# Kernel tuning notes

Hardware: AMD Instinct MI355X
Metric: run time of the kernel (lower is better)

## Reference

```python
import jax, jax.numpy as jnp
import numpy as np

EPS = 1e-6

def setup_inputs() -> dict:
    key = jax.random.key(0)
    ks = jax.random.split(key, 4)
    T, B, D, N = 512, 16, 1024, 512
    # xavier-uniform-ish scale for projections
    lim = float(np.sqrt(6.0 / (N + D)))
    x = jax.random.normal(ks[0], (T, B, D), dtype=jnp.float32)
    W_k = jax.random.uniform(ks[1], (N, D), minval=-lim, maxval=lim, dtype=jnp.float32)
    W_v = jax.random.uniform(ks[2], (N, D), minval=-lim, maxval=lim, dtype=jnp.float32)
    W_q = jax.random.uniform(ks[3], (N, D), minval=-lim, maxval=lim, dtype=jnp.float32)
    return {"x": x, "W_k": W_k, "W_v": W_v, "W_q": W_q}

def reference(x, W_k, W_v, W_q):
    # x: (T, B, D); delta-rule fast-weight cell, proj=no_z, nonlin=tanh,
    # gate=output, update=delta.
    T, B, D = x.shape
    n = W_k.shape[0]
    k = jnp.einsum('tbd,nd->tbn', x, W_k)
    v = jnp.einsum('tbd,nd->tbn', x, W_v)
    q = jnp.einsum('tbd,nd->tbn', x, W_q)
    k_norm = k / (jnp.linalg.norm(k, axis=-1, keepdims=True) + EPS)

    def step(S, kvq):
        k_t, v_t, q_t = kvq  # each (B, n)
        retrieved = jnp.einsum('bij,bj->bi', S, k_t)
        delta = v_t - retrieved
        S_new = jnp.tanh(S + delta[:, :, None] * k_t[:, None, :])
        Sq = jnp.einsum('bij,bj->bi', S_new, q_t)
        out = Sq * jax.nn.silu(Sq)
        return S_new, out

    S0 = jnp.zeros((B, n, n), dtype=x.dtype)
    S_final, outputs = jax.lax.scan(step, S0, (k_norm, v, q))
    return outputs, S_final
```

## Files before the change

### kernel.cpp

```cpp
#include <hip/hip_runtime.h>
#include <hip/hip_bf16.h>

#define T_DIM 512
#define B_DIM 16
#define D_DIM 1024
#define N_DIM 512

#define C_FOLD  2.885390082f
#define INV_C   0.3465735903f

typedef short s16x8 __attribute__((ext_vector_type(8)));
typedef float f32x4 __attribute__((ext_vector_type(4)));
typedef float f32x2 __attribute__((ext_vector_type(2)));

__device__ __forceinline__ unsigned short f2bf(float f) {
    unsigned u = __float_as_uint(f);
    unsigned r = (u + 0x7fffu + ((u >> 16) & 1u)) >> 16;
    return (unsigned short)r;
}

__device__ __forceinline__ float half32_sum(float x) {
    x += __int_as_float(__builtin_amdgcn_update_dpp(0, __float_as_int(x), 0xB1,  0xf, 0xf, true));
    x += __int_as_float(__builtin_amdgcn_update_dpp(0, __float_as_int(x), 0x4E,  0xf, 0xf, true));
    x += __int_as_float(__builtin_amdgcn_update_dpp(0, __float_as_int(x), 0x124, 0xf, 0xf, true));
    x += __int_as_float(__builtin_amdgcn_update_dpp(0, __float_as_int(x), 0x128, 0xf, 0xf, true));
    x += __int_as_float(__builtin_amdgcn_ds_swizzle(__float_as_int(x), 0x401F));
    return x;
}

__global__ __launch_bounds__(256) void proj_gemm(
    const float* __restrict__ x,
    const float* __restrict__ Wk,
    const float* __restrict__ Wv,
    const float* __restrict__ Wq,
    float* __restrict__ kbuf, float* __restrict__ vbuf, float* __restrict__ qbuf)
{
    const float* W = (blockIdx.z == 0) ? Wk : (blockIdx.z == 1) ? Wv : Wq;
    float* out = (blockIdx.z == 0) ? kbuf : (blockIdx.z == 1) ? vbuf : qbuf;

    __shared__ __align__(16) unsigned short As[64 * 40];
    __shared__ __align__(16) unsigned short Bs[64 * 40];

    const int tid  = threadIdx.x;
    const int m0   = blockIdx.x * 64;
    const int n0   = blockIdx.y * 64;
    const int wave = tid >> 6;
    const int lane = tid & 63;
    const int l15  = lane & 15;
    const int quad = lane >> 4;

    const int srow = tid >> 2;
    const int scol = (tid & 3) * 8;

    f32x4 acc[4];
#pragma unroll
    for (int i = 0; i < 4; ++i) acc[i] = (f32x4)0.0f;

    for (int k0 = 0; k0 < D_DIM; k0 += 32) {
        __syncthreads();
        {
            const float* srcA = &x[(size_t)(m0 + srow) * D_DIM + k0 + scol];
            float4 a0 = *(const float4*)srcA;
            float4 a1 = *(const float4*)(srcA + 4);
            uint4 pa;
            pa.x = (unsigned)f2bf(a0.x) | ((unsigned)f2bf(a0.y) << 16);
            pa.y = (unsigned)f2bf(a0.z) | ((unsigned)f2bf(a0.w) << 16);
            pa.z = (unsigned)f2bf(a1.x) | ((unsigned)f2bf(a1.y) << 16);
            pa.w = (unsigned)f2bf(a1.z) | ((unsigned)f2bf(a1.w) << 16);
            *(uint4*)&As[srow * 40 + scol] = pa;

            const float* srcB = &W[(size_t)(n0 + srow) * D_DIM + k0 + scol];
            float4 b0 = *(const float4*)srcB;
            float4 b1 = *(const float4*)(srcB + 4);
            uint4 pb;
            pb.x = (unsigned)f2bf(b0.x) | ((unsigned)f2bf(b0.y) << 16);
            pb.y = (unsigned)f2bf(b0.z) | ((unsigned)f2bf(b0.w) << 16);
            pb.z = (unsigned)f2bf(b1.x) | ((unsigned)f2bf(b1.y) << 16);
            pb.w = (unsigned)f2bf(b1.z) | ((unsigned)f2bf(b1.w) << 16);
            *(uint4*)&Bs[srow * 40 + scol] = pb;
        }
        __syncthreads();
        s16x8 af = *(const s16x8*)&As[(wave * 16 + l15) * 40 + quad * 8];
#pragma unroll
        for (int nt = 0; nt < 4; ++nt) {
            s16x8 bf = *(const s16x8*)&Bs[(nt * 16 + l15) * 40 + quad * 8];
            acc[nt] = __builtin_amdgcn_mfma_f32_16x16x32_bf16(af, bf, acc[nt], 0, 0, 0);
        }
    }
#pragma unroll
    for (int nt = 0; nt < 4; ++nt) {
#pragma unroll
        for (int rg = 0; rg < 4; ++rg) {
            int row = m0 + wave * 16 + quad * 4 + rg;
            int col = n0 + nt * 16 + l15;
            out[(size_t)row * N_DIM + col] = acc[nt][rg];
        }
    }
}

__global__ __launch_bounds__(256) void knorm(float* __restrict__ kbuf)
{
    const int wave = threadIdx.x >> 6;
    const int lane = threadIdx.x & 63;
    const int row  = blockIdx.x * 4 + wave;
    float* p = &kbuf[(size_t)row * N_DIM + lane * 8];
    float4 a = *(const float4*)p;
    float4 b = *(const float4*)(p + 4);
    float s = a.x*a.x + a.y*a.y + a.z*a.z + a.w*a.w
            + b.x*b.x + b.y*b.y + b.z*b.z + b.w*b.w;
#pragma unroll
    for (int m = 1; m < 64; m <<= 1) s += __shfl_xor(s, m, 64);
    float inv = 1.0f / (sqrtf(s) + 1e-6f);
    a.x *= inv; a.y *= inv; a.z *= inv; a.w *= inv;
    b.x *= inv; b.y *= inv; b.z *= inv; b.w *= inv;
    *(float4*)p = a;
    *(float4*)(p + 4) = b;
}

__global__ __launch_bounds__(256) void scan_kernel(
    const float* __restrict__ kbuf, const float* __restrict__ vbuf,
    const float* __restrict__ qbuf, float* __restrict__ out)
{
    __shared__ __align__(16) float ks[2][576];
    __shared__ __align__(16) float qs[2][576];
    __shared__ float vs[2][16];

    const int tid  = threadIdx.x;
    const int lane = tid & 63;
    const int wv   = tid >> 6;
    const int h    = lane >> 5;
    const int tj   = lane & 31;
    const int b    = blockIdx.y;
    const int i0   = blockIdx.x * 16;
    const int r0   = 4 * wv + 2 * h;

    const int wA = 18 * (tid >> 3) + ((2 * tid) & 15);
    const int rA = 18 * tj;

    f32x2 SA[8], SB[8];
#pragma unroll
    for (int u = 0; u < 8; ++u) { SA[u] = (f32x2)0.0f; SB[u] = (f32x2)0.0f; }

    float2 pk, pq; float pv = 0.0f;
    {
        const size_t o0 = (size_t)b * N_DIM;
        pk = *(const float2*)&kbuf[o0 + 2 * tid];
        pq = *(const float2*)&qbuf[o0 + 2 * tid];
        if (tid < 16) pv = vbuf[o0 + i0 + tid];
        *(float2*)&ks[0][wA] = pk;
        *(float2*)&qs[0][wA] = pq;
        if (tid < 16) vs[0][tid] = pv;
        const size_t o1 = (size_t)(B_DIM + b) * N_DIM;
        pk = *(const float2*)&kbuf[o1 + 2 * tid];
        pq = *(const float2*)&qbuf[o1 + 2 * tid];
        if (tid < 16) pv = vbuf[o1 + i0 + tid];
    }
    __syncthreads();

    const f32x2 Cv   = {C_FOLD, C_FOLD};
    const f32x2 M2Cv = {-2.0f * C_FOLD, -2.0f * C_FOLD};

    for (int t = 0; t < T_DIM; ++t) {
        const int cb = t & 1, nb = cb ^ 1;
        const size_t ofs = ((size_t)t * B_DIM + b) * N_DIM;

        if (t + 1 < T_DIM) {
            *(float2*)&ks[nb][wA] = pk;
            *(float2*)&qs[nb][wA] = pq;
            if (tid < 16) vs[nb][tid] = pv;
        }
        if (t + 2 < T_DIM) {
            const size_t o2 = ((size_t)(t + 2) * B_DIM + b) * N_DIM;
            pk = *(const float2*)&kbuf[o2 + 2 * tid];
            pq = *(const float2*)&qbuf[o2 + 2 * tid];
            if (tid < 16) pv = vbuf[o2 + i0 + tid];
        }

        f32x2 k2[8], q2[8];
#pragma unroll
        for (int u = 0; u < 8; ++u) {
            k2[u] = *(const f32x2*)&ks[cb][rA + 2 * u];
            q2[u] = *(const f32x2*)&qs[cb][rA + 2 * u];
        }
        const float v0 = vs[cb][r0];
        const float v1 = vs[cb][r0 + 1];

        f32x2 pa0 = (f32x2)0.0f, pb0 = (f32x2)0.0f;
        f32x2 pa1 = (f32x2)0.0f, pb1 = (f32x2)0.0f;
#pragma unroll
        for (int u = 0; u < 8; u += 2) {
            pa0 += SA[u] * k2[u];  pb0 += SA[u + 1] * k2[u + 1];
            pa1 += SB[u] * k2[u];  pb1 += SB[u + 1] * k2[u + 1];
        }
        const float racc0 = half32_sum(pa0.x + pa0.y + pb0.x + pb0.y);
        const float racc1 = half32_sum(pa1.x + pa1.y + pb1.x + pb1.y);

        const float dp0 = __builtin_fmaf(C_FOLD, v0, -racc0);
        const float dp1 = __builtin_fmaf(C_FOLD, v1, -racc1);
        const f32x2 d0 = {dp0, dp0}, d1 = {dp1, dp1};

        f32x2 sa0 = (f32x2)0.0f, sb0 = (f32x2)0.0f;
        f32x2 sa1 = (f32x2)0.0f, sb1 = (f32x2)0.0f;
#pragma unroll
        for (int u = 0; u < 8; ++u) {
            f32x2 argA = SA[u] + d0 * k2[u];
            f32x2 argB = SB[u] + d1 * k2[u];
            f32x2 eA = { __builtin_amdgcn_exp2f(argA.x), __builtin_amdgcn_exp2f(argA.y) };
            f32x2 eB = { __builtin_amdgcn_exp2f(argB.x), __builtin_amdgcn_exp2f(argB.y) };
            eA = eA + 1.0f; eB = eB + 1.0f;
            f32x2 rrA = { __builtin_amdgcn_rcpf(eA.x), __builtin_amdgcn_rcpf(eA.y) };
            f32x2 rrB = { __builtin_amdgcn_rcpf(eB.x), __builtin_amdgcn_rcpf(eB.y) };
            f32x2 snA = Cv + rrA * M2Cv;
            f32x2 snB = Cv + rrB * M2Cv;
            SA[u] = snA; SB[u] = snB;
            if (u & 1) { sb0 += snA * q2[u]; sb1 += snB * q2[u]; }
            else       { sa0 += snA * q2[u]; sa1 += snB * q2[u]; }
        }
        const float sq0 = half32_sum(sa0.x + sa0.y + sb0.x + sb0.y);
        const float sq1 = half32_sum(sa1.x + sa1.y + sb1.x + sb1.y);

        if (tj == 0) {
            float s0 = sq0 * INV_C, s1 = sq1 * INV_C;
            float g0 = __builtin_amdgcn_rcpf(1.0f + __builtin_amdgcn_exp2f(-s0 * 1.44269504f));
            float g1 = __builtin_amdgcn_rcpf(1.0f + __builtin_amdgcn_exp2f(-s1 * 1.44269504f));
            out[ofs + i0 + r0]     = s0 * s0 * g0;
            out[ofs + i0 + r0 + 1] = s1 * s1 * g1;
        }
        __syncthreads();
    }

    const size_t base = (size_t)T_DIM * B_DIM * N_DIM;
    const size_t so0 = base + ((size_t)b * N_DIM + i0 + r0) * N_DIM + 16 * tj;
    const size_t so1 = so0 + N_DIM;
#pragma unroll
    for (int u = 0; u < 4; ++u) {
        float4 w0, w1;
        w0.x = SA[2*u].x   * INV_C; w0.y = SA[2*u].y   * INV_C;
        w0.z = SA[2*u+1].x * INV_C; w0.w = SA[2*u+1].y * INV_C;
        w1.x = SB[2*u].x   * INV_C; w1.y = SB[2*u].y   * INV_C;
        w1.z = SB[2*u+1].x * INV_C; w1.w = SB[2*u+1].y * INV_C;
        *(float4*)&out[so0 + 4 * u] = w0;
        *(float4*)&out[so1 + 4 * u] = w1;
    }
}

extern "C" void kernel_launch(void* const* d_in, const int* in_sizes, int n_in,
                              void* d_out, int out_size, void* d_ws, size_t ws_size,
                              hipStream_t stream) {
    const float* x  = (const float*)d_in[0];
    const float* Wk = (const float*)d_in[1];
    const float* Wv = (const float*)d_in[2];
    const float* Wq = (const float*)d_in[3];
    float* outp = (float*)d_out;

    const size_t MN = (size_t)T_DIM * B_DIM * N_DIM;
    float* kbuf = (float*)d_ws;
    float* vbuf = kbuf + MN;
    float* qbuf = vbuf + MN;

    proj_gemm<<<dim3(128, 8, 3), 256, 0, stream>>>(x, Wk, Wv, Wq, kbuf, vbuf, qbuf);
    knorm<<<2048, 256, 0, stream>>>(kbuf);
    scan_kernel<<<dim3(32, 16), 256, 0, stream>>>(kbuf, vbuf, qbuf, outp);
}
```

Measured before the change: 795.8 us.

## Repartition scan so each wave owns full rows with wave-wide DPP reductions

The scan kernel is remapped so each wave holds two full state rows spread across all 64 lanes, 8 columns per lane. Before, each half-wave held two rows with 16 columns per lane. Blocks now cover 8 rows instead of 16, which doubles the grid to 1024 blocks, and launch bounds ask for 4 blocks per CU to raise occupancy. The row reductions become full-wave DPP row_shr/row_bcast sums finished with a readlane. This halves per-thread state and LDS padding, but adds longer reductions and more blocks each re-reading k/q per step.

Measured after the change: 951.9 us. 1.2x slower.

```diff
diff --git a/kernel.cpp b/kernel.cpp
--- a/kernel.cpp
+++ b/kernel.cpp
@@ -11,7 +11,6 @@
 
 typedef short s16x8 __attribute__((ext_vector_type(8)));
 typedef float f32x4 __attribute__((ext_vector_type(4)));
-typedef float f32x2 __attribute__((ext_vector_type(2)));
 
 __device__ __forceinline__ unsigned short f2bf(float f) {
     unsigned u = __float_as_uint(f);
@@ -19,12 +18,19 @@
     return (unsigned short)r;
 }
 
-__device__ __forceinline__ float half32_sum(float x) {
-    x += __int_as_float(__builtin_amdgcn_update_dpp(0, __float_as_int(x), 0xB1,  0xf, 0xf, true));
-    x += __int_as_float(__builtin_amdgcn_update_dpp(0, __float_as_int(x), 0x4E,  0xf, 0xf, true));
-    x += __int_as_float(__builtin_amdgcn_update_dpp(0, __float_as_int(x), 0x124, 0xf, 0xf, true));
-    x += __int_as_float(__builtin_amdgcn_update_dpp(0, __float_as_int(x), 0x128, 0xf, 0xf, true));
-    x += __int_as_float(__builtin_amdgcn_ds_swizzle(__float_as_int(x), 0x401F));
+template <int CTRL, int RMASK>
+__device__ __forceinline__ float dpp_add(float x) {
+    return x + __int_as_float(__builtin_amdgcn_update_dpp(
+        0, __float_as_int(x), CTRL, RMASK, 0xf, true));
+}
+
+__device__ __forceinline__ float wave_sum_lane63(float x) {
+    x = dpp_add<0x111, 0xf>(x);
+    x = dpp_add<0x112, 0xf>(x);
+    x = dpp_add<0x114, 0xf>(x);
+    x = dpp_add<0x118, 0xf>(x);
+    x = dpp_add<0x142, 0xa>(x);
+    x = dpp_add<0x143, 0xc>(x);
     return x;
 }
 
@@ -117,131 +123,127 @@
     *(float4*)(p + 4) = b;
 }
 
-__global__ __launch_bounds__(256) void scan_kernel(
+__global__ __launch_bounds__(256, 4) void scan_kernel(
     const float* __restrict__ kbuf, const float* __restrict__ vbuf,
     const float* __restrict__ qbuf, float* __restrict__ out)
 {
-    __shared__ __align__(16) float ks[2][576];
-    __shared__ __align__(16) float qs[2][576];
-    __shared__ float vs[2][16];
+    __shared__ __align__(16) float ks[2][512];
+    __shared__ __align__(16) float qs[2][512];
+    __shared__ float vs[2][8];
 
     const int tid  = threadIdx.x;
-    const int lane = tid & 63;
-    const int wv   = tid >> 6;
-    const int h    = lane >> 5;
-    const int tj   = lane & 31;
+    const int w    = tid >> 6;
+    const int L    = tid & 63;
     const int b    = blockIdx.y;
-    const int i0   = blockIdx.x * 16;
-    const int r0   = 4 * wv + 2 * h;
-
-    const int wA = 18 * (tid >> 3) + ((2 * tid) & 15);
-    const int rA = 18 * tj;
-
-    f32x2 SA[8], SB[8];
-#pragma unroll
-    for (int u = 0; u < 8; ++u) { SA[u] = (f32x2)0.0f; SB[u] = (f32x2)0.0f; }
+    const int i0   = blockIdx.x * 8;
+    const int row0 = 2 * w;
+    const int c0   = 8 * L;
+
+    float S0[8], S1[8];
+#pragma unroll
+    for (int u = 0; u < 8; ++u) { S0[u] = 0.0f; S1[u] = 0.0f; }
 
     float2 pk, pq; float pv = 0.0f;
     {
         const size_t o0 = (size_t)b * N_DIM;
         pk = *(const float2*)&kbuf[o0 + 2 * tid];
         pq = *(const float2*)&qbuf[o0 + 2 * tid];
-        if (tid < 16) pv = vbuf[o0 + i0 + tid];
-        *(float2*)&ks[0][wA] = pk;
-        *(float2*)&qs[0][wA] = pq;
-        if (tid < 16) vs[0][tid] = pv;
+        if (tid < 8) pv = vbuf[o0 + i0 + tid];
+        *(float2*)&ks[0][2 * tid] = pk;
+        *(float2*)&qs[0][2 * tid] = pq;
+        if (tid < 8) vs[0][tid] = pv;
         const size_t o1 = (size_t)(B_DIM + b) * N_DIM;
         pk = *(const float2*)&kbuf[o1 + 2 * tid];
         pq = *(const float2*)&qbuf[o1 + 2 * tid];
-        if (tid < 16) pv = vbuf[o1 + i0 + tid];
+        if (tid < 8) pv = vbuf[o1 + i0 + tid];
     }
     __syncthreads();
-
-    const f32x2 Cv   = {C_FOLD, C_FOLD};
-    const f32x2 M2Cv = {-2.0f * C_FOLD, -2.0f * C_FOLD};
 
     for (int t = 0; t < T_DIM; ++t) {
         const int cb = t & 1, nb = cb ^ 1;
         const size_t ofs = ((size_t)t * B_DIM + b) * N_DIM;
 
         if (t + 1 < T_DIM) {
-            *(float2*)&ks[nb][wA] = pk;
-            *(float2*)&qs[nb][wA] = pq;
-            if (tid < 16) vs[nb][tid] = pv;
+            *(float2*)&ks[nb][2 * tid] = pk;
+            *(float2*)&qs[nb][2 * tid] = pq;
+            if (tid < 8) vs[nb][tid] = pv;
         }
         if (t + 2 < T_DIM) {
             const size_t o2 = ((size_t)(t + 2) * B_DIM + b) * N_DIM;
             pk = *(const float2*)&kbuf[o2 + 2 * tid];
             pq = *(const float2*)&qbuf[o2 + 2 * tid];
-            if (tid < 16) pv = vbuf[o2 + i0 + tid];
-        }
-
-        f32x2 k2[8], q2[8];
-#pragma unroll
-        for (int u = 0; u < 8; ++u) {
-            k2[u] = *(const f32x2*)&ks[cb][rA + 2 * u];
-            q2[u] = *(const f32x2*)&qs[cb][rA + 2 * u];
-        }
-        const float v0 = vs[cb][r0];
-        const float v1 = vs[cb][r0 + 1];
-
-        f32x2 pa0 = (f32x2)0.0f, pb0 = (f32x2)0.0f;
-        f32x2 pa1 = (f32x2)0.0f, pb1 = (f32x2)0.0f;
-#pragma unroll
-        for (int u = 0; u < 8; u += 2) {
-            pa0 += SA[u] * k2[u];  pb0 += SA[u + 1] * k2[u + 1];
-            pa1 += SB[u] * k2[u];  pb1 += SB[u + 1] * k2[u + 1];
-        }
-        const float racc0 = half32_sum(pa0.x + pa0.y + pb0.x + pb0.y);
-        const float racc1 = half32_sum(pa1.x + pa1.y + pb1.x + pb1.y);
+            if (tid < 8) pv = vbuf[o2 + i0 + tid];
+        }
+
+        float kk[8], qq[8];
+        {
+            f32x4 k0v = *(const f32x4*)&ks[cb][c0];
+            f32x4 k1v = *(const f32x4*)&ks[cb][c0 + 4];
+            f32x4 q0v = *(const f32x4*)&qs[cb][c0];
+            f32x4 q1v = *(const f32x4*)&qs[cb][c0 + 4];
+#pragma unroll
+            for (int u = 0; u < 4; ++u) {
+                kk[u] = k0v[u]; kk[u + 4] = k1v[u];
+                qq[u] = q0v[u]; qq[u + 4] = q1v[u];
+            }
+        }
+        const float v0 = vs[cb][row0];
+        const float v1 = vs[cb][row0 + 1];
+
+        float a0 = 0.f, a1 = 0.f, b0 = 0.f, b1 = 0.f;
+#pragma unroll
+        for (int u = 0; u < 4; ++u) {
+            a0 = __builtin_fmaf(S0[u],     kk[u],     a0);
+            a1 = __builtin_fmaf(S0[u + 4], kk[u + 4], a1);
+            b0 = __builtin_fmaf(S1[u],     kk[u],     b0);
+            b1 = __builtin_fmaf(S1[u + 4], kk[u + 4], b1);
+        }
+        float red0 = wave_sum_lane63(a0 + a1);
+        float red1 = wave_sum_lane63(b0 + b1);
+        const float racc0 = __int_as_float(__builtin_amdgcn_readlane(__float_as_int(red0), 63));
+        const float racc1 = __int_as_float(__builtin_amdgcn_readlane(__float_as_int(red1), 63));
 
         const float dp0 = __builtin_fmaf(C_FOLD, v0, -racc0);
         const float dp1 = __builtin_fmaf(C_FOLD, v1, -racc1);
-        const f32x2 d0 = {dp0, dp0}, d1 = {dp1, dp1};
-
-        f32x2 sa0 = (f32x2)0.0f, sb0 = (f32x2)0.0f;
-        f32x2 sa1 = (f32x2)0.0f, sb1 = (f32x2)0.0f;
+
+        float s0a = 0.f, s0b = 0.f, s1a = 0.f, s1b = 0.f;
 #pragma unroll
         for (int u = 0; u < 8; ++u) {
-            f32x2 argA = SA[u] + d0 * k2[u];
-            f32x2 argB = SB[u] + d1 * k2[u];
-            f32x2 eA = { __builtin_amdgcn_exp2f(argA.x), __builtin_amdgcn_exp2f(argA.y) };
-            f32x2 eB = { __builtin_amdgcn_exp2f(argB.x), __builtin_amdgcn_exp2f(argB.y) };
-            eA = eA + 1.0f; eB = eB + 1.0f;
-            f32x2 rrA = { __builtin_amdgcn_rcpf(eA.x), __builtin_amdgcn_rcpf(eA.y) };
-            f32x2 rrB = { __builtin_amdgcn_rcpf(eB.x), __builtin_amdgcn_rcpf(eB.y) };
-            f32x2 snA = Cv + rrA * M2Cv;
-            f32x2 snB = Cv + rrB * M2Cv;
-            SA[u] = snA; SB[u] = snB;
-            if (u & 1) { sb0 += snA * q2[u]; sb1 += snB * q2[u]; }
-            else       { sa0 += snA * q2[u]; sa1 += snB * q2[u]; }
-        }
-        const float sq0 = half32_sum(sa0.x + sa0.y + sb0.x + sb0.y);
-        const float sq1 = half32_sum(sa1.x + sa1.y + sb1.x + sb1.y);
-
-        if (tj == 0) {
-            float s0 = sq0 * INV_C, s1 = sq1 * INV_C;
-            float g0 = __builtin_amdgcn_rcpf(1.0f + __builtin_amdgcn_exp2f(-s0 * 1.44269504f));
-            float g1 = __builtin_amdgcn_rcpf(1.0f + __builtin_amdgcn_exp2f(-s1 * 1.44269504f));
-            out[ofs + i0 + r0]     = s0 * s0 * g0;
-            out[ofs + i0 + r0 + 1] = s1 * s1 * g1;
+            float g0 = __builtin_fmaf(dp0, kk[u], S0[u]);
+            float g1 = __builtin_fmaf(dp1, kk[u], S1[u]);
+            float e0 = __builtin_amdgcn_exp2f(g0) + 1.0f;
+            float e1 = __builtin_amdgcn_exp2f(g1) + 1.0f;
+            float n0 = __builtin_fmaf(-2.0f * C_FOLD, __builtin_amdgcn_rcpf(e0), C_FOLD);
+            float n1 = __builtin_fmaf(-2.0f * C_FOLD, __builtin_amdgcn_rcpf(e1), C_FOLD);
+            S0[u] = n0; S1[u] = n1;
+            if (u & 1) { s0b = __builtin_fmaf(n0, qq[u], s0b); s1b = __builtin_fmaf(n1, qq[u], s1b); }
+            else       { s0a = __builtin_fmaf(n0, qq[u], s0a); s1a = __builtin_fmaf(n1, qq[u], s1a); }
+        }
+        float sq0 = wave_sum_lane63(s0a + s0b);
+        float sq1 = wave_sum_lane63(s1a + s1b);
+
+        if (L == 63) {
+            float t0 = sq0 * INV_C, t1 = sq1 * INV_C;
+            float g0 = __builtin_amdgcn_rcpf(1.0f + __builtin_amdgcn_exp2f(-t0 * 1.44269504f));
+            float g1 = __builtin_amdgcn_rcpf(1.0f + __builtin_amdgcn_exp2f(-t1 * 1.44269504f));
+            float2 o2; o2.x = t0 * t0 * g0; o2.y = t1 * t1 * g1;
+            *(float2*)&out[ofs + i0 + row0] = o2;
         }
         __syncthreads();
     }
 
     const size_t base = (size_t)T_DIM * B_DIM * N_DIM;
-    const size_t so0 = base + ((size_t)b * N_DIM + i0 + r0) * N_DIM + 16 * tj;
+    const size_t so0 = base + ((size_t)b * N_DIM + i0 + row0) * N_DIM + c0;
     const size_t so1 = so0 + N_DIM;
-#pragma unroll
-    for (int u = 0; u < 4; ++u) {
-        float4 w0, w1;
-        w0.x = SA[2*u].x   * INV_C; w0.y = SA[2*u].y   * INV_C;
-        w0.z = SA[2*u+1].x * INV_C; w0.w = SA[2*u+1].y * INV_C;
-        w1.x = SB[2*u].x   * INV_C; w1.y = SB[2*u].y   * INV_C;
-        w1.z = SB[2*u+1].x * INV_C; w1.w = SB[2*u+1].y * INV_C;
-        *(float4*)&out[so0 + 4 * u] = w0;
-        *(float4*)&out[so1 + 4 * u] = w1;
-    }
+    float4 w0, w1;
+    w0.x = S0[0] * INV_C; w0.y = S0[1] * INV_C; w0.z = S0[2] * INV_C; w0.w = S0[3] * INV_C;
+    *(float4*)&out[so0] = w0;
+    w0.x = S0[4] * INV_C; w0.y = S0[5] * INV_C; w0.z = S0[6] * INV_C; w0.w = S0[7] * INV_C;
+    *(float4*)&out[so0 + 4] = w0;
+    w1.x = S1[0] * INV_C; w1.y = S1[1] * INV_C; w1.z = S1[2] * INV_C; w1.w = S1[3] * INV_C;
+    *(float4*)&out[so1] = w1;
+    w1.x = S1[4] * INV_C; w1.y = S1[5] * INV_C; w1.z = S1[6] * INV_C; w1.w = S1[7] * INV_C;
+    *(float4*)&out[so1 + 4] = w1;
 }
 
 extern "C" void kernel_launch(void* const* d_in, const int* in_sizes, int n_in,
@@ -260,5 +262,5 @@
 
     proj_gemm<<<dim3(128, 8, 3), 256, 0, stream>>>(x, Wk, Wv, Wq, kbuf, vbuf, qbuf);
     knorm<<<2048, 256, 0, stream>>>(kbuf);
-    scan_kernel<<<dim3(32, 16), 256, 0, stream>>>(kbuf, vbuf, qbuf, outp);
-}
+    scan_kernel<<<dim3(64, 16), 256, 0, stream>>>(kbuf, vbuf, qbuf, outp);
+}
```
